# Kernel tuning notes

Hardware: AMD Instinct MI355X
Metric: run time of the kernel (lower is better)

The kernel has to match this reference:

```python
import jax, jax.numpy as jnp
import numpy as np
from jax import lax

B, C, H, W = 2, 64, 128, 128
F_SCALE, STRIDE = 2, 2
F = F_SCALE * STRIDE            # pixel-unshuffle factor = 4
CK = C // 16                    # attention channel dim = 4
SCALE_DIM = C // F_SCALE        # softmax scale uses embed_size//f_scale = 32


def setup_inputs() -> dict:
    key = jax.random.key(0)
    ks = jax.random.split(key, 16)
    g = lambda i, shape, s=0.05: jax.random.normal(ks[i], shape, jnp.float32) * s
    return {
        "x":   jax.random.normal(ks[0], (B, C, H, W), jnp.float32),
        # conv1 = Sequential(1x1 C->CK, 1x1 CK->CK)
        "w1a": g(1, (CK, C)), "b1a": g(2, (CK,)),
        "w1b": g(3, (CK, CK)), "b1b": g(4, (CK,)),
        # wqk parameter (torch.randn, std 1)
        "wqk": jax.random.normal(ks[5], (CK, CK), jnp.float32),
        # conv2: 1x1 CK->C ; conv: 1x1 C->C
        "w2":  g(6, (C, CK)), "b2": g(7, (C,)),
        "wc":  g(8, (C, C)), "bc": g(9, (C,)),
        # FF (GridSANaive): 1x1 C->C/4, 3x3 dilated C/4->C/4, 1x1 C/4->C
        "wf1": g(10, (C // 4, C)), "bf1": g(11, (C // 4,)),
        "wf2": g(12, (C // 4, C // 4, 3, 3)), "bf2": g(13, (C // 4,)),
        "wf3": g(14, (C, C // 4)), "bf3": g(15, (C,)),
    }


def conv1x1(x, w, b):
    return jnp.einsum('bchw,oc->bohw', x, w) + b[None, :, None, None]


def grid_attention(x, wqk):
    b, c, h, w = x.shape
    sh = h // 2
    x = jnp.pad(x, ((0, 0), (0, 0), (sh, 0), (0, 0)))      # Shift2d pad (top)
    # F.layer_norm over last 3 dims, no affine, eps=1e-5
    mu = jnp.mean(x, axis=(1, 2, 3), keepdims=True)
    var = jnp.var(x, axis=(1, 2, 3), keepdims=True)
    xx = (x - mu) / jnp.sqrt(var + 1e-5)
    hh, ww = xx.shape[2], xx.shape[3]
    ph, pw = (F - hh % F) % F, (F - ww % F) % F
    xx = jnp.pad(xx, ((0, 0), (0, 0), (0, ph), (0, pw)))
    gh, gw = (hh + ph) // F, (ww + pw) // F
    # pixel_unshuffle: channel layout (c, fy, fx)
    xx = xx.reshape(b, c, gh, F, gw, F).transpose(0, 1, 3, 5, 2, 4)
    xx = xx.reshape(b, c * F * F, gh, gw)
    # rearrange 'b (f c) h w -> (b f) c h w', f=F*F (mixes layout, as in original)
    xx = xx.reshape(b * F * F, c, gh, gw)
    L = gh * gw
    tok = xx.transpose(0, 2, 3, 1).reshape(b * F * F, L, c)   # (bg, L, c)
    qk = tok @ wqk
    qk = qk / (jnp.linalg.norm(qk, axis=-1, keepdims=True) + 1e-8)
    attn = (jnp.einsum('blk,bmk->blm', qk, qk) + 1.0) / (SCALE_DIM ** 0.5)
    attn = jax.nn.softmax(attn, axis=-1)
    out = jnp.einsum('blm,bmc->blc', attn, tok)
    out = out.reshape(b * F * F, gh, gw, c).transpose(0, 3, 1, 2)
    out = out.reshape(b, F * F * c, gh, gw)
    # pixel_shuffle: channel layout (fy, fx, c)
    out = out.reshape(b, F, F, c, gh, gw).transpose(0, 3, 4, 1, 5, 2)
    out = out.reshape(b, c, gh * F, gw * F)
    out = out[:, :, :hh, :ww]                               # undo shuffle pad
    return out[:, :, :-sh, :] if sh > 0 else out            # Shift2d crop (bottom)


def ff(x, wf1, bf1, wf2, bf2, wf3, bf3):
    h1 = jax.nn.relu(conv1x1(x, wf1, bf1))
    k = 1 + (STRIDE // 2) * 2   # ShiftConv2d offset for 3x3, dilation=STRIDE
    hp = jnp.pad(h1, ((0, 0), (0, 0), (k, 0), (0, 0)))
    h2 = lax.conv_general_dilated(
        hp, wf2, (1, 1), ((STRIDE, STRIDE), (STRIDE, STRIDE)),
        rhs_dilation=(STRIDE, STRIDE),
        dimension_numbers=('NCHW', 'OIHW', 'NCHW'))
    h2 = jax.nn.relu((h2 + bf2[None, :, None, None])[:, :, :-k, :])
    return conv1x1(h2, wf3, bf3)


def reference(x, w1a, b1a, w1b, b1b, wqk, w2, b2, wc, bc,
              wf1, bf1, wf2, bf2, wf3, bf3):
    a = conv1x1(conv1x1(x, w1a, b1a), w1b, b1b)
    att = grid_attention(a, wqk)
    y = x + conv1x1(conv1x1(att, w2, b2), wc, bc)
    return y + ff(y, wf1, bf1, wf2, bf2, wf3, bf3)
```

## Files before the change

### kernel.cpp

```cpp
#include <hip/hip_runtime.h>
#include <math.h>

#define CHW  (64*16384)
#define ATT_SCALE 0.17677669529663687f

__global__ __launch_bounds__(256) void k1_a_stats(
    const float* __restrict__ x, const float* __restrict__ w1a,
    const float* __restrict__ b1a, const float* __restrict__ w1b,
    const float* __restrict__ b1b, float* __restrict__ a,
    float* __restrict__ statsbuf) {
  __shared__ float sA[256];
  __shared__ float sb1[4];
  __shared__ float pc[4][4][256];
  __shared__ float rs[64], rq[64];
  int tid = threadIdx.x;
  {
    int o = tid >> 6, c = tid & 63;
    float s = 0.f;
    #pragma unroll
    for (int k = 0; k < 4; ++k) s += w1b[o*4+k] * w1a[k*64+c];
    sA[tid] = s;
  }
  if (tid < 4) {
    float s = b1b[tid];
    #pragma unroll
    for (int k = 0; k < 4; ++k) s += w1b[tid*4+k] * b1a[k];
    sb1[tid] = s;
  }
  __syncthreads();
  int quad = tid & 15, cg = tid >> 4;
  int gq = blockIdx.x * 16 + quad;
  int bb = gq >> 12;
  int px0 = (gq & 4095) * 4;
  const float* xp = x + bb*CHW + (cg*4)*16384 + px0;
  float4 acc[4];
  #pragma unroll
  for (int o = 0; o < 4; ++o) acc[o] = make_float4(0.f,0.f,0.f,0.f);
  #pragma unroll
  for (int cc = 0; cc < 4; ++cc) {
    float4 xv = *(const float4*)(xp + cc*16384);
    int c = cg*4 + cc;
    #pragma unroll
    for (int o = 0; o < 4; ++o) {
      float w = sA[o*64+c];
      acc[o].x += w*xv.x; acc[o].y += w*xv.y; acc[o].z += w*xv.z; acc[o].w += w*xv.w;
    }
  }
  #pragma unroll
  for (int o = 0; o < 4; ++o) {
    pc[0][o][tid] = acc[o].x; pc[1][o][tid] = acc[o].y;
    pc[2][o][tid] = acc[o].z; pc[3][o][tid] = acc[o].w;
  }
  __syncthreads();
  if (tid < 64) {
    int q2 = tid & 15, o = tid >> 4;
    float sx=0.f, sy=0.f, sz=0.f, sw=0.f;
    #pragma unroll
    for (int g2 = 0; g2 < 16; ++g2) {
      int idx = g2*16 + q2;
      sx += pc[0][o][idx]; sy += pc[1][o][idx];
      sz += pc[2][o][idx]; sw += pc[3][o][idx];
    }
    float bv = sb1[o];
    sx += bv; sy += bv; sz += bv; sw += bv;
    int gq2 = blockIdx.x*16 + q2;
    int b2 = gq2 >> 12; int p0 = (gq2 & 4095)*4;
    *(float4*)(a + b2*4*16384 + o*16384 + p0) = make_float4(sx,sy,sz,sw);
    rs[tid] = sx+sy+sz+sw;
    rq[tid] = sx*sx+sy*sy+sz*sz+sw*sw;
  }
  __syncthreads();
  for (int s2 = 32; s2; s2 >>= 1) {
    if (tid < s2) { rs[tid] += rs[tid+s2]; rq[tid] += rq[tid+s2]; }
    __syncthreads();
  }
  if (tid == 0) { statsbuf[blockIdx.x*2] = rs[0]; statsbuf[blockIdx.x*2+1] = rq[0]; }
}

__global__ __launch_bounds__(256) void k2_tok_qk(
    const float* __restrict__ a, const float* __restrict__ statsbuf,
    const float* __restrict__ wqk, float4* __restrict__ tok,
    float4* __restrict__ qko) {
  __shared__ float rs[256], rq[256];
  int tid = threadIdx.x;
  int g = blockIdx.x / 6;
  int t = (blockIdx.x % 6) * 256 + tid;
  int b = g >> 4, u = (g >> 2) & 3, v = g & 3;
  rs[tid] = statsbuf[(b*256+tid)*2];
  rq[tid] = statsbuf[(b*256+tid)*2+1];
  __syncthreads();
  for (int s2 = 128; s2; s2 >>= 1) {
    if (tid < s2) { rs[tid] += rs[tid+s2]; rq[tid] += rq[tid+s2]; }
    __syncthreads();
  }
  float mu  = rs[0] * (1.f/98304.f);
  float var = rq[0] * (1.f/98304.f) - mu*mu;
  float rsig = rsqrtf(var + 1e-5f);
  int i = t >> 5, j = t & 31;
  int Hp = i*4 + v;
  float4 tv;
  if (Hp >= 64) {
    tv = *(const float4*)(a + (b*4+u)*16384 + (Hp-64)*128 + j*4);
    tv.x = (tv.x-mu)*rsig; tv.y = (tv.y-mu)*rsig;
    tv.z = (tv.z-mu)*rsig; tv.w = (tv.w-mu)*rsig;
  } else {
    float z = -mu*rsig;
    tv = make_float4(z,z,z,z);
  }
  float q0 = tv.x*wqk[0] + tv.y*wqk[4] + tv.z*wqk[8]  + tv.w*wqk[12];
  float q1 = tv.x*wqk[1] + tv.y*wqk[5] + tv.z*wqk[9]  + tv.w*wqk[13];
  float q2 = tv.x*wqk[2] + tv.y*wqk[6] + tv.z*wqk[10] + tv.w*wqk[14];
  float q3 = tv.x*wqk[3] + tv.y*wqk[7] + tv.z*wqk[11] + tv.w*wqk[15];
  float nrm = sqrtf(q0*q0 + q1*q1 + q2*q2 + q3*q3);
  float inv = 1.f / (nrm + 1e-8f);
  int idx = g*1536 + t;
  tok[idx] = tv;
  qko[idx] = make_float4(q0*inv, q1*inv, q2*inv, q3*inv);
}

__device__ __forceinline__ float poly_exp(float d) {
  return 1.f + d*(1.f + d*(0.5f + d*(0.16666667f + d*0.04166667f)));
}
__global__ __launch_bounds__(512) void k3_attn(
    const float4* __restrict__ tok, const float4* __restrict__ qk,
    float* __restrict__ att) {
  __shared__ float4 kq[1024];
  __shared__ float4 kt[1024];
  __shared__ float red[16][5][128];
  int tid = threadIdx.x;
  int g = blockIdx.x >> 3, qb = blockIdx.x & 7;
  const float4* qg = qk  + g*1536;
  const float4* tg = tok + g*1536;
  for (int m = tid; m < 1024; m += 512) { kq[m] = qg[512+m]; kt[m] = tg[512+m]; }
  __syncthreads();
  int qi = tid & 31, s = tid >> 5;
  int t0 = qb*128 + qi*4;
  float4 q[4];
  #pragma unroll
  for (int j = 0; j < 4; ++j) {
    float4 v = qg[t0+j];
    q[j] = make_float4(v.x*ATT_SCALE, v.y*ATT_SCALE, v.z*ATT_SCALE, v.w*ATT_SCALE);
  }
  float den[4] = {0.f,0.f,0.f,0.f};
  float4 ov[4];
  #pragma unroll
  for (int j = 0; j < 4; ++j) ov[j] = make_float4(0.f,0.f,0.f,0.f);
  if (s == 0) {
    float4 k0 = qg[0]; float4 tv0 = tg[0];
    #pragma unroll
    for (int j = 0; j < 4; ++j) {
      float d = q[j].x*k0.x + q[j].y*k0.y + q[j].z*k0.z + q[j].w*k0.w;
      float e = 512.f * poly_exp(d);
      den[j] += e;
      ov[j].x += e*tv0.x; ov[j].y += e*tv0.y; ov[j].z += e*tv0.z; ov[j].w += e*tv0.w;
    }
  }
  int m0 = s * 64;
  #pragma unroll 2
  for (int m = m0; m < m0 + 64; ++m) {
    float4 kk = kq[m];
    float4 tv = kt[m];
    #pragma unroll
    for (int j = 0; j < 4; ++j) {
      float d = q[j].x*kk.x + q[j].y*kk.y + q[j].z*kk.z + q[j].w*kk.w;
      float e = poly_exp(d);
      den[j] += e;
      ov[j].x += e*tv.x; ov[j].y += e*tv.y; ov[j].z += e*tv.z; ov[j].w += e*tv.w;
    }
  }
  #pragma unroll
  for (int j = 0; j < 4; ++j) {
    int key = j*32 + qi;
    red[s][0][key] = den[j];
    red[s][1][key] = ov[j].x; red[s][2][key] = ov[j].y;
    red[s][3][key] = ov[j].z; red[s][4][key] = ov[j].w;
  }
  __syncthreads();
  if (tid < 128) {
    int qi_r = tid & 31, j_r = tid >> 5;
    float dsum=0.f, ox=0.f, oy=0.f, oz=0.f, ow=0.f;
    #pragma unroll
    for (int ss = 0; ss < 16; ++ss) {
      dsum += red[ss][0][tid];
      ox += red[ss][1][tid]; oy += red[ss][2][tid];
      oz += red[ss][3][tid]; ow += red[ss][4][tid];
    }
    float inv = 1.f / dsum;
    int t = qb*128 + qi_r*4 + j_r;
    int b = g >> 4, u = (g >> 2) & 3, v = g & 3;
    int i = t >> 5, j = t & 31;
    float* ap = att + b*4*16384 + (i*4+u)*128 + (j*4+v);
    ap[0]     = ox*inv;
    ap[16384] = oy*inv;
    ap[32768] = oz*inv;
    ap[49152] = ow*inv;
  }
}

__global__ __launch_bounds__(512) void k4_y_h1(
    const float* __restrict__ x, const float* __restrict__ att,
    const float* __restrict__ w2p, const float* __restrict__ b2p,
    const float* __restrict__ wcp, const float* __restrict__ bcp,
    const float* __restrict__ wf1, const float* __restrict__ bf1,
    float* __restrict__ yout, float* __restrict__ h1) {
  __shared__ float sWf[64][4];
  __shared__ float sbf[64];
  __shared__ float sw1[1024];
  __shared__ float sb1[16];
  __shared__ float4 satt[4][32];
  __shared__ float4 ylds[64][32];
  int tid = threadIdx.x;
  if (tid < 256) {
    int o = tid >> 2, k = tid & 3;
    float s = 0.f;
    for (int c = 0; c < 64; ++c) s += wcp[o*64+c] * w2p[c*4+k];
    sWf[o][k] = s;
  }
  if (tid < 64) {
    float s = bcp[tid];
    for (int c = 0; c < 64; ++c) s += wcp[tid*64+c] * b2p[c];
    sbf[tid] = s;
  }
  for (int i = tid; i < 1024; i += 512) sw1[i] = wf1[i];
  if (tid < 16) sb1[tid] = bf1[tid];
  int quad = tid & 31, og = tid >> 5;
  int gq = blockIdx.x*32 + quad;
  int bb = gq >> 12; int px0 = (gq & 4095)*4;
  if (tid < 128) {
    int k = tid >> 5, q2 = tid & 31;
    int gq2 = blockIdx.x*32 + q2;
    int b2i = gq2 >> 12; int p0 = (gq2 & 4095)*4;
    satt[k][q2] = *(const float4*)(att + b2i*4*16384 + k*16384 + p0);
  }
  __syncthreads();
  float4 a0 = satt[0][quad], a1 = satt[1][quad], a2 = satt[2][quad], a3 = satt[3][quad];
  const float* xp = x + bb*CHW + px0;
  float* yp = yout + bb*CHW + px0;
  #pragma unroll
  for (int cc = 0; cc < 4; ++cc) {
    int c = og*4 + cc;
    float4 xv = *(const float4*)(xp + c*16384);
    float w0 = sWf[c][0], w1 = sWf[c][1], w2v = sWf[c][2], w3 = sWf[c][3];
    float bv = sbf[c];
    float4 yv;
    yv.x = xv.x + w0*a0.x + w1*a1.x + w2v*a2.x + w3*a3.x + bv;
    yv.y = xv.y + w0*a0.y + w1*a1.y + w2v*a2.y + w3*a3.y + bv;
    yv.z = xv.z + w0*a0.z + w1*a1.z + w2v*a2.z + w3*a3.z + bv;
    yv.w = xv.w + w0*a0.w + w1*a1.w + w2v*a2.w + w3*a3.w + bv;
    *(float4*)(yp + c*16384) = yv;
    ylds[c][quad] = yv;
  }
  __syncthreads();
  float bv = sb1[og];
  float4 acc = make_float4(bv, bv, bv, bv);
  #pragma unroll 8
  for (int c = 0; c < 64; ++c) {
    float4 yv = ylds[c][quad];
    float wa = sw1[og*64+c];
    acc.x += wa*yv.x; acc.y += wa*yv.y; acc.z += wa*yv.z; acc.w += wa*yv.w;
  }
  acc.x = fmaxf(acc.x,0.f); acc.y = fmaxf(acc.y,0.f);
  acc.z = fmaxf(acc.z,0.f); acc.w = fmaxf(acc.w,0.f);
  *(float4*)(h1 + bb*16*16384 + og*16384 + px0) = acc;
}

__global__ __launch_bounds__(512) void k6_ff_out(
    const float* __restrict__ h1, const float* __restrict__ wf2,
    const float* __restrict__ bf2, const float* __restrict__ wf3,
    const float* __restrict__ bf3, float* yo) {
  __shared__ float sbuf[16][3][136];
  __shared__ float h2buf[128][21];
  int tid = threadIdx.x;
  int bb = blockIdx.x >> 7, h = blockIdx.x & 127;
  for (int idx = tid; idx < 16*3*136; idx += 512) {
    int c = idx / (3*136);
    int r = (idx / 136) % 3;
    int col = idx % 136;
    int row = h - 5 + 2*r;
    int w = col - 4;
    float v = 0.f;
    if (row >= 0 && w >= 0 && w < 128)
      v = h1[bb*16*16384 + c*16384 + row*128 + w];
    sbuf[c][r][col] = v;
  }
  __syncthreads();
  int w = tid & 127;
  int g = __builtin_amdgcn_readfirstlane(tid >> 7);
  float acc[4];
  #pragma unroll
  for (int o = 0; o < 4; ++o) acc[o] = bf2[g*4+o];
  #pragma unroll 4
  for (int c = 0; c < 16; ++c) {
    #pragma unroll
    for (int r = 0; r < 3; ++r) {
      float tm2 = sbuf[c][r][w+2];
      float t00 = sbuf[c][r][w+4];
      float tp2 = sbuf[c][r][w+6];
      #pragma unroll
      for (int o = 0; o < 4; ++o) {
        const float* wp = wf2 + (((g*4+o)*16 + c)*3 + r)*3;
        acc[o] += wp[0]*tm2 + wp[1]*t00 + wp[2]*tp2;
      }
    }
  }
  #pragma unroll
  for (int o = 0; o < 4; ++o) h2buf[w][g*4+o] = fmaxf(acc[o], 0.f);
  __syncthreads();
  float hv[16];
  #pragma unroll
  for (int k = 0; k < 16; ++k) hv[k] = h2buf[w][k];
  float* ybase = yo + bb*CHW + h*128 + w;
  #pragma unroll 4
  for (int oc = 0; oc < 16; ++oc) {
    int o = g*16 + oc;
    float sv = bf3[o] + ybase[o*16384];
    #pragma unroll
    for (int k = 0; k < 16; ++k) sv += wf3[o*16+k]*hv[k];
    ybase[o*16384] = sv;
  }
}

extern "C" void kernel_launch(void* const* d_in, const int* in_sizes, int n_in,
                              void* d_out, int out_size, void* d_ws, size_t ws_size,
                              hipStream_t stream) {
  (void)in_sizes; (void)n_in; (void)out_size; (void)ws_size;
  const float* x   = (const float*)d_in[0];
  const float* w1a = (const float*)d_in[1];
  const float* b1a = (const float*)d_in[2];
  const float* w1b = (const float*)d_in[3];
  const float* b1b = (const float*)d_in[4];
  const float* wqk = (const float*)d_in[5];
  const float* w2  = (const float*)d_in[6];
  const float* b2  = (const float*)d_in[7];
  const float* wc  = (const float*)d_in[8];
  const float* bc  = (const float*)d_in[9];
  const float* wf1 = (const float*)d_in[10];
  const float* bf1 = (const float*)d_in[11];
  const float* wf2 = (const float*)d_in[12];
  const float* bf2 = (const float*)d_in[13];
  const float* wf3 = (const float*)d_in[14];
  const float* bf3 = (const float*)d_in[15];

  float* ws = (float*)d_ws;
  float*  a_    = ws;
  float*  stats = ws + 131072;
  float4* tok   = (float4*)(ws + 132096);
  float4* qkb   = (float4*)(ws + 328704);
  float*  att   = ws + 525312;
  float*  h1    = ws + 656384;
  float*  y     = (float*)d_out;

  k1_a_stats<<<512, 256, 0, stream>>>(x, w1a, b1a, w1b, b1b, a_, stats);
  k2_tok_qk <<<192, 256, 0, stream>>>(a_, stats, wqk, tok, qkb);
  k3_attn   <<<256, 512, 0, stream>>>(tok, qkb, att);
  k4_y_h1   <<<256, 512, 0, stream>>>(x, att, w2, b2, wc, bc, wf1, bf1, y, h1);
  k6_ff_out <<<256, 512, 0, stream>>>(h1, wf2, bf2, wf3, bf3, y);
}
```

Baseline: 135.2 us.

## Fuse token normalization and qk projection into attention kernel, specialize padded query rows

Removes the separate tok/qk kernel. The attention kernel now reduces the layer-norm stats itself with wavefront shuffles, normalizes and projects its 1024 real keys directly into shared memory, and computes the padded-row key analytically. Query blocks that fall entirely in the zero-padded region share one constant query, so they are computed once per block with a tree reduction instead of the full per-query loop. This saves one launch and the global round trip of tok/qk. In exchange, every block redundantly recomputes the key projection for its group.

```diff
diff --git a/kernel.cpp b/kernel.cpp
--- a/kernel.cpp
+++ b/kernel.cpp
@@ -77,123 +77,165 @@
   if (tid == 0) { statsbuf[blockIdx.x*2] = rs[0]; statsbuf[blockIdx.x*2+1] = rq[0]; }
 }
 
-__global__ __launch_bounds__(256) void k2_tok_qk(
-    const float* __restrict__ a, const float* __restrict__ statsbuf,
-    const float* __restrict__ wqk, float4* __restrict__ tok,
-    float4* __restrict__ qko) {
-  __shared__ float rs[256], rq[256];
-  int tid = threadIdx.x;
-  int g = blockIdx.x / 6;
-  int t = (blockIdx.x % 6) * 256 + tid;
-  int b = g >> 4, u = (g >> 2) & 3, v = g & 3;
-  rs[tid] = statsbuf[(b*256+tid)*2];
-  rq[tid] = statsbuf[(b*256+tid)*2+1];
-  __syncthreads();
-  for (int s2 = 128; s2; s2 >>= 1) {
-    if (tid < s2) { rs[tid] += rs[tid+s2]; rq[tid] += rq[tid+s2]; }
-    __syncthreads();
-  }
-  float mu  = rs[0] * (1.f/98304.f);
-  float var = rq[0] * (1.f/98304.f) - mu*mu;
-  float rsig = rsqrtf(var + 1e-5f);
-  int i = t >> 5, j = t & 31;
-  int Hp = i*4 + v;
-  float4 tv;
-  if (Hp >= 64) {
-    tv = *(const float4*)(a + (b*4+u)*16384 + (Hp-64)*128 + j*4);
-    tv.x = (tv.x-mu)*rsig; tv.y = (tv.y-mu)*rsig;
-    tv.z = (tv.z-mu)*rsig; tv.w = (tv.w-mu)*rsig;
-  } else {
-    float z = -mu*rsig;
-    tv = make_float4(z,z,z,z);
-  }
-  float q0 = tv.x*wqk[0] + tv.y*wqk[4] + tv.z*wqk[8]  + tv.w*wqk[12];
-  float q1 = tv.x*wqk[1] + tv.y*wqk[5] + tv.z*wqk[9]  + tv.w*wqk[13];
-  float q2 = tv.x*wqk[2] + tv.y*wqk[6] + tv.z*wqk[10] + tv.w*wqk[14];
-  float q3 = tv.x*wqk[3] + tv.y*wqk[7] + tv.z*wqk[11] + tv.w*wqk[15];
-  float nrm = sqrtf(q0*q0 + q1*q1 + q2*q2 + q3*q3);
-  float inv = 1.f / (nrm + 1e-8f);
-  int idx = g*1536 + t;
-  tok[idx] = tv;
-  qko[idx] = make_float4(q0*inv, q1*inv, q2*inv, q3*inv);
-}
-
 __device__ __forceinline__ float poly_exp(float d) {
   return 1.f + d*(1.f + d*(0.5f + d*(0.16666667f + d*0.04166667f)));
 }
 __global__ __launch_bounds__(512) void k3_attn(
-    const float4* __restrict__ tok, const float4* __restrict__ qk,
-    float* __restrict__ att) {
+    const float* __restrict__ a, const float* __restrict__ statsbuf,
+    const float* __restrict__ wqk, float* __restrict__ att) {
   __shared__ float4 kq[1024];
   __shared__ float4 kt[1024];
   __shared__ float red[16][5][128];
+  __shared__ float sred[8];
   int tid = threadIdx.x;
   int g = blockIdx.x >> 3, qb = blockIdx.x & 7;
-  const float4* qg = qk  + g*1536;
-  const float4* tg = tok + g*1536;
-  for (int m = tid; m < 1024; m += 512) { kq[m] = qg[512+m]; kt[m] = tg[512+m]; }
-  __syncthreads();
-  int qi = tid & 31, s = tid >> 5;
-  int t0 = qb*128 + qi*4;
-  float4 q[4];
-  #pragma unroll
-  for (int j = 0; j < 4; ++j) {
-    float4 v = qg[t0+j];
-    q[j] = make_float4(v.x*ATT_SCALE, v.y*ATT_SCALE, v.z*ATT_SCALE, v.w*ATT_SCALE);
-  }
-  float den[4] = {0.f,0.f,0.f,0.f};
-  float4 ov[4];
-  #pragma unroll
-  for (int j = 0; j < 4; ++j) ov[j] = make_float4(0.f,0.f,0.f,0.f);
-  if (s == 0) {
-    float4 k0 = qg[0]; float4 tv0 = tg[0];
+  int b = g >> 4, u = (g >> 2) & 3, v = g & 3;
+
+  if (tid < 256) {
+    float2 p = ((const float2*)statsbuf)[b*256 + tid];
+    float vs = p.x, vq = p.y;
+    #pragma unroll
+    for (int off = 32; off; off >>= 1) {
+      vs += __shfl_down(vs, off); vq += __shfl_down(vq, off);
+    }
+    if ((tid & 63) == 0) { sred[tid>>6] = vs; sred[4 + (tid>>6)] = vq; }
+  }
+  __syncthreads();
+  float mu  = (sred[0]+sred[1]+sred[2]+sred[3]) * (1.f/98304.f);
+  float var = (sred[4]+sred[5]+sred[6]+sred[7]) * (1.f/98304.f) - mu*mu;
+  float rsig = rsqrtf(var + 1e-5f);
+
+  const float* ap = a + (b*4+u)*16384;
+  for (int m = tid; m < 1024; m += 512) {
+    int t = 512 + m;
+    int i = t >> 5, j = m & 31;
+    float4 tv = *(const float4*)(ap + (i*4 + v - 64)*128 + j*4);
+    tv.x = (tv.x-mu)*rsig; tv.y = (tv.y-mu)*rsig;
+    tv.z = (tv.z-mu)*rsig; tv.w = (tv.w-mu)*rsig;
+    float q0 = tv.x*wqk[0] + tv.y*wqk[4] + tv.z*wqk[8]  + tv.w*wqk[12];
+    float q1 = tv.x*wqk[1] + tv.y*wqk[5] + tv.z*wqk[9]  + tv.w*wqk[13];
+    float q2 = tv.x*wqk[2] + tv.y*wqk[6] + tv.z*wqk[10] + tv.w*wqk[14];
+    float q3 = tv.x*wqk[3] + tv.y*wqk[7] + tv.z*wqk[11] + tv.w*wqk[15];
+    float inv = 1.f / (sqrtf(q0*q0 + q1*q1 + q2*q2 + q3*q3) + 1e-8f);
+    kq[m] = make_float4(q0*inv, q1*inv, q2*inv, q3*inv);
+    kt[m] = tv;
+  }
+  float z = -mu*rsig;
+  float4 t0tv = make_float4(z, z, z, z);
+  float p0 = z*(wqk[0] + wqk[4] + wqk[8]  + wqk[12]);
+  float p1 = z*(wqk[1] + wqk[5] + wqk[9]  + wqk[13]);
+  float p2 = z*(wqk[2] + wqk[6] + wqk[10] + wqk[14]);
+  float p3 = z*(wqk[3] + wqk[7] + wqk[11] + wqk[15]);
+  float inv0 = 1.f / (sqrtf(p0*p0 + p1*p1 + p2*p2 + p3*p3) + 1e-8f);
+  float4 t0qk = make_float4(p0*inv0, p1*inv0, p2*inv0, p3*inv0);
+  __syncthreads();
+
+  if (qb >= 4) {
+    int qi = tid & 31, s = tid >> 5;
+    int t0 = (qb - 4)*128 + qi*4;
+    float4 q[4];
     #pragma unroll
     for (int j = 0; j < 4; ++j) {
-      float d = q[j].x*k0.x + q[j].y*k0.y + q[j].z*k0.z + q[j].w*k0.w;
+      float4 vq = kq[t0 + j];
+      q[j] = make_float4(vq.x*ATT_SCALE, vq.y*ATT_SCALE, vq.z*ATT_SCALE, vq.w*ATT_SCALE);
+    }
+    float den[4] = {0.f,0.f,0.f,0.f};
+    float4 ov[4];
+    #pragma unroll
+    for (int j = 0; j < 4; ++j) ov[j] = make_float4(0.f,0.f,0.f,0.f);
+    if (s == 0) {
+      #pragma unroll
+      for (int j = 0; j < 4; ++j) {
+        float d = q[j].x*t0qk.x + q[j].y*t0qk.y + q[j].z*t0qk.z + q[j].w*t0qk.w;
+        float e = 512.f * poly_exp(d);
+        den[j] += e;
+        ov[j].x += e*t0tv.x; ov[j].y += e*t0tv.y; ov[j].z += e*t0tv.z; ov[j].w += e*t0tv.w;
+      }
+    }
+    int m0 = s * 64;
+    #pragma unroll 2
+    for (int m = m0; m < m0 + 64; ++m) {
+      float4 kk = kq[m];
+      float4 tv = kt[m];
+      #pragma unroll
+      for (int j = 0; j < 4; ++j) {
+        float d = q[j].x*kk.x + q[j].y*kk.y + q[j].z*kk.z + q[j].w*kk.w;
+        float e = poly_exp(d);
+        den[j] += e;
+        ov[j].x += e*tv.x; ov[j].y += e*tv.y; ov[j].z += e*tv.z; ov[j].w += e*tv.w;
+      }
+    }
+    #pragma unroll
+    for (int j = 0; j < 4; ++j) {
+      int key = j*32 + qi;
+      red[s][0][key] = den[j];
+      red[s][1][key] = ov[j].x; red[s][2][key] = ov[j].y;
+      red[s][3][key] = ov[j].z; red[s][4][key] = ov[j].w;
+    }
+    __syncthreads();
+    if (tid < 128) {
+      int qi_r = tid & 31, j_r = tid >> 5;
+      float dsum=0.f, ox=0.f, oy=0.f, oz=0.f, ow=0.f;
+      #pragma unroll
+      for (int ss = 0; ss < 16; ++ss) {
+        dsum += red[ss][0][tid];
+        ox += red[ss][1][tid]; oy += red[ss][2][tid];
+        oz += red[ss][3][tid]; ow += red[ss][4][tid];
+      }
+      float inv = 1.f / dsum;
+      int t = qb*128 + qi_r*4 + j_r;
+      int i = t >> 5, j = t & 31;
+      float* ap2 = att + b*4*16384 + (i*4+u)*128 + (j*4+v);
+      ap2[0]     = ox*inv;
+      ap2[16384] = oy*inv;
+      ap2[32768] = oz*inv;
+      ap2[49152] = ow*inv;
+    }
+  } else {
+    float4 qs = make_float4(t0qk.x*ATT_SCALE, t0qk.y*ATT_SCALE,
+                            t0qk.z*ATT_SCALE, t0qk.w*ATT_SCALE);
+    float den = 0.f; float4 ov = make_float4(0.f,0.f,0.f,0.f);
+    #pragma unroll
+    for (int mm = 0; mm < 2; ++mm) {
+      int m = tid*2 + mm;
+      float4 kk = kq[m];
+      float4 tv = kt[m];
+      float d = qs.x*kk.x + qs.y*kk.y + qs.z*kk.z + qs.w*kk.w;
+      float e = poly_exp(d);
+      den += e;
+      ov.x += e*tv.x; ov.y += e*tv.y; ov.z += e*tv.z; ov.w += e*tv.w;
+    }
+    if (tid == 0) {
+      float d = qs.x*t0qk.x + qs.y*t0qk.y + qs.z*t0qk.z + qs.w*t0qk.w;
       float e = 512.f * poly_exp(d);
-      den[j] += e;
-      ov[j].x += e*tv0.x; ov[j].y += e*tv0.y; ov[j].z += e*tv0.z; ov[j].w += e*tv0.w;
-    }
-  }
-  int m0 = s * 64;
-  #pragma unroll 2
-  for (int m = m0; m < m0 + 64; ++m) {
-    float4 kk = kq[m];
-    float4 tv = kt[m];
-    #pragma unroll
-    for (int j = 0; j < 4; ++j) {
-      float d = q[j].x*kk.x + q[j].y*kk.y + q[j].z*kk.z + q[j].w*kk.w;
-      float e = poly_exp(d);
-      den[j] += e;
-      ov[j].x += e*tv.x; ov[j].y += e*tv.y; ov[j].z += e*tv.z; ov[j].w += e*tv.w;
-    }
-  }
-  #pragma unroll
-  for (int j = 0; j < 4; ++j) {
-    int key = j*32 + qi;
-    red[s][0][key] = den[j];
-    red[s][1][key] = ov[j].x; red[s][2][key] = ov[j].y;
-    red[s][3][key] = ov[j].z; red[s][4][key] = ov[j].w;
-  }
-  __syncthreads();
-  if (tid < 128) {
-    int qi_r = tid & 31, j_r = tid >> 5;
-    float dsum=0.f, ox=0.f, oy=0.f, oz=0.f, ow=0.f;
-    #pragma unroll
-    for (int ss = 0; ss < 16; ++ss) {
-      dsum += red[ss][0][tid];
-      ox += red[ss][1][tid]; oy += red[ss][2][tid];
-      oz += red[ss][3][tid]; ow += red[ss][4][tid];
-    }
-    float inv = 1.f / dsum;
-    int t = qb*128 + qi_r*4 + j_r;
-    int b = g >> 4, u = (g >> 2) & 3, v = g & 3;
+      den += e;
+      ov.x += e*t0tv.x; ov.y += e*t0tv.y; ov.z += e*t0tv.z; ov.w += e*t0tv.w;
+    }
+    float* sc = &red[0][0][0];
+    sc[tid]        = den;
+    sc[512 + tid]  = ov.x;
+    sc[1024 + tid] = ov.y;
+    sc[1536 + tid] = ov.z;
+    sc[2048 + tid] = ov.w;
+    __syncthreads();
+    for (int s2 = 256; s2; s2 >>= 1) {
+      if (tid < s2) {
+        sc[tid]        += sc[tid + s2];
+        sc[512 + tid]  += sc[512 + tid + s2];
+        sc[1024 + tid] += sc[1024 + tid + s2];
+        sc[1536 + tid] += sc[1536 + tid + s2];
+        sc[2048 + tid] += sc[2048 + tid + s2];
+      }
+      __syncthreads();
+    }
+    float invd = 1.f / sc[0];
+    float res0 = sc[512]*invd, res1 = sc[1024]*invd,
+          res2 = sc[1536]*invd, res3 = sc[2048]*invd;
+    int comp = tid >> 7, tloc = tid & 127;
+    int t = qb*128 + tloc;
     int i = t >> 5, j = t & 31;
-    float* ap = att + b*4*16384 + (i*4+u)*128 + (j*4+v);
-    ap[0]     = ox*inv;
-    ap[16384] = oy*inv;
-    ap[32768] = oz*inv;
-    ap[49152] = ow*inv;
+    float val = (comp == 0) ? res0 : (comp == 1) ? res1 : (comp == 2) ? res2 : res3;
+    att[b*4*16384 + comp*16384 + (i*4+u)*128 + (j*4+v)] = val;
   }
 }
 
@@ -344,15 +386,12 @@
   float* ws = (float*)d_ws;
   float*  a_    = ws;
   float*  stats = ws + 131072;
-  float4* tok   = (float4*)(ws + 132096);
-  float4* qkb   = (float4*)(ws + 328704);
   float*  att   = ws + 525312;
   float*  h1    = ws + 656384;
   float*  y     = (float*)d_out;
 
   k1_a_stats<<<512, 256, 0, stream>>>(x, w1a, b1a, w1b, b1b, a_, stats);
-  k2_tok_qk <<<192, 256, 0, stream>>>(a_, stats, wqk, tok, qkb);
-  k3_attn   <<<256, 512, 0, stream>>>(tok, qkb, att);
+  k3_attn   <<<256, 512, 0, stream>>>(a_, stats, wqk, att);
   k4_y_h1   <<<256, 512, 0, stream>>>(x, att, w2, b2, wc, bc, wf1, bf1, y, h1);
   k6_ff_out <<<256, 512, 0, stream>>>(h1, wf2, bf2, wf3, bf3, y);
 }
```

After: 130.9 us. 1.03x faster.
